# Kernel tuning notes

Hardware: AMD Instinct MI355X
Metric: run time of the kernel (lower is better)

Reference implementation:

```python
import jax, jax.numpy as jnp
from jax import lax
import numpy as np

RADIUS = 0.2
NSAMPLE = 64


def _ball_query(xyz, new_xyz, radius, nsample):
    """Faithful PointNet++ ball query.

    For each center, take the first `nsample` point indices (in index order)
    whose squared distance < radius^2; if fewer than nsample are found, the
    remaining slots are filled with the first found index (CUDA kernel
    semantics). Returns int32 idx of shape (B, npoint, nsample).
    """
    N = xyz.shape[1]
    # (B, npoint, N) squared distances
    d2 = jnp.sum((new_xyz[:, :, None, :] - xyz[:, None, :, :]) ** 2, axis=-1)
    within = d2 < (radius * radius)
    # key = point index if within ball, else N (sentinel); smallest nsample
    # keys == first nsample in-ball indices in index order.
    key = jnp.where(within, jnp.arange(N, dtype=jnp.int32), jnp.int32(N))
    neg_vals, _ = lax.top_k(-key, nsample)          # largest of -key = smallest key
    sel = -neg_vals                                  # (B, npoint, nsample)
    valid = sel < N
    first = jnp.where(valid[..., :1], sel[..., :1], 0)  # first found idx (or 0)
    return jnp.where(valid, sel, first)


def _group_gather(features, idx):
    # features: (B, C, N), idx: (B, npoint, nsample) -> (B, C, npoint, nsample)
    return jax.vmap(lambda f, i: f[:, i])(features, idx)


def setup_inputs() -> dict:
    key = jax.random.key(0)
    k1, k2, k3 = jax.random.split(key, 3)
    B, N, npoint, C = 4, 16384, 2048, 64
    xyz = jax.random.uniform(k1, (B, N, 3), dtype=jnp.float32)
    new_xyz = jax.random.uniform(k2, (B, npoint, 3), dtype=jnp.float32)
    features = jax.random.normal(k3, (B, C, N), dtype=jnp.float32)
    return {"xyz": xyz, "new_xyz": new_xyz, "features": features}


def reference(xyz, new_xyz, features):
    idx = _ball_query(xyz, new_xyz, RADIUS, NSAMPLE)          # (B, npoint, nsample)
    xyz_t = jnp.transpose(xyz, (0, 2, 1))                      # (B, 3, N)
    grouped_xyz = _group_gather(xyz_t, idx)                    # (B, 3, npoint, nsample)
    grouped_xyz = grouped_xyz - jnp.transpose(new_xyz, (0, 2, 1))[..., None]
    grouped_features = _group_gather(features, idx)            # (B, C, npoint, nsample)
    new_features = jnp.concatenate([grouped_xyz, grouped_features], axis=1)
    # original code does .transpose(1, 2) -> (B, npoint, 3+C, nsample)
    return jnp.transpose(new_features, (0, 2, 1, 3))
```

## Files before the change

kernel.cpp:

```cpp
#include <hip/hip_runtime.h>


#define BB 4
#define NN 16384
#define NP 2048
#define CC 64
#define NS 64
#define CH (3 + CC)
#define NCHUNK (NN / 256)
#define ST 65

typedef float f32x4 __attribute__((ext_vector_type(4)));

__global__ __launch_bounds__(256) void pn2_transpose_kernel(
    const float* __restrict__ f, float* __restrict__ ft)
{
    __shared__ float tile[CC][65];
    const int g = blockIdx.x;
    const int xcd = g & 7;
    const int b = xcd >> 1;
    const int tidx = ((xcd & 1) << 7) + (g >> 3);
    const int n0 = tidx << 6;
    const int col = threadIdx.x & 63;
    const int r4  = threadIdx.x >> 6;
    const float* src = f + (size_t)b * CC * NN;
#pragma unroll
    for (int i = 0; i < 16; ++i) {
        const int c = r4 + i * 4;
        tile[c][col] = __builtin_nontemporal_load(&src[(size_t)c * NN + n0 + col]);
    }
    __syncthreads();
    float* dst = ft + ((size_t)b * NN + n0) * CC;
#pragma unroll
    for (int i = 0; i < 16; ++i) {
        const int n = r4 + i * 4;
        dst[(size_t)n * CC + col] = tile[col][n];
    }
}

__global__ __launch_bounds__(256, 4) void pn2_qg_kernel(
    const float* __restrict__ xyz,
    const float* __restrict__ new_xyz,
    const float* __restrict__ ft,
    float* __restrict__ out)
{
    __shared__ int sidx[4][NS];
    __shared__ float stile[4][32 * ST];

    const int lane = threadIdx.x & 63;
    const int wave = threadIdx.x >> 6;

    const int g = blockIdx.x;
    const int xcd = g & 7;
    const int cg = ((xcd >> 1) << 9) + ((xcd & 1) << 8) + (g >> 3);
    const int center = cg * 4 + wave;
    const int b = center >> 11;
    const int j = center & (NP - 1);

    const float r2 = 0.04f;
    const float* q = new_xyz + ((size_t)b * NP + j) * 3;
    const float cx = q[0], cy = q[1], cz = q[2];

    const float* xb = xyz + (size_t)b * NN * 3;
    const float4* x4 = (const float4*)xb;
    int* widx = sidx[wave];

    const int base = 3 * lane;
    const unsigned long long low = (1ull << lane) - 1ull;
    int found = 0;
    int it = 0;
    float4 A = x4[base], Bv = x4[base + 1], Cv = x4[base + 2];

    while (true) {
        const int nit = (it + 1 < NCHUNK) ? it + 1 : it;
        const size_t nb = (size_t)nit * 192 + base;
        float4 nA = x4[nb], nB = x4[nb + 1], nC = x4[nb + 2];

        const int n0 = it * 256 + 4 * lane;
        const float px[4] = {A.x, A.w, Bv.z, Cv.y};
        const float py[4] = {A.y, Bv.x, Bv.w, Cv.z};
        const float pz[4] = {A.z, Bv.y, Cv.x, Cv.w};
        bool in[4];
        unsigned long long m[4];
#pragma unroll
        for (int k = 0; k < 4; ++k) {
            const float dx = px[k] - cx;
            const float dy = py[k] - cy;
            const float dz = pz[k] - cz;
            const float d2 = __fadd_rn(__fadd_rn(__fmul_rn(dx, dx), __fmul_rn(dy, dy)),
                                       __fmul_rn(dz, dz));
            in[k] = d2 < r2;
            m[k] = __ballot(in[k]);
        }
        int pos = found
                + (int)__popcll(m[0] & low) + (int)__popcll(m[1] & low)
                + (int)__popcll(m[2] & low) + (int)__popcll(m[3] & low);
#pragma unroll
        for (int k = 0; k < 4; ++k) {
            if (in[k]) {
                if (pos < NS) widx[pos] = n0 + k;
                ++pos;
            }
        }
        found += (int)(__popcll(m[0]) + __popcll(m[1])
                     + __popcll(m[2]) + __popcll(m[3]));
        if (found >= NS || it == NCHUNK - 1) break;
        A = nA; Bv = nB; Cv = nC; ++it;
    }

    int myidx = 0;
    if (found > 0) {
        const int first = widx[0];
        myidx = (lane < found) ? widx[lane] : first;
    }
    widx[lane] = myidx;

    const float* pp = xb + (size_t)myidx * 3;
    float* ob = out + (size_t)center * CH * NS;
    __builtin_nontemporal_store(pp[0] - cx, ob + 0 * NS + lane);
    __builtin_nontemporal_store(pp[1] - cy, ob + 1 * NS + lane);
    __builtin_nontemporal_store(pp[2] - cz, ob + 2 * NS + lane);

    const float* ftb = ft + (size_t)b * NN * CC;
    float* tw = stile[wave];
    const int sub  = lane & 15;
    const int rsub = lane >> 4;
    const int sq   = lane & 7;
    const int cc8  = lane >> 3;

#pragma unroll
    for (int h = 0; h < 2; ++h) {
        int ridx[8];
#pragma unroll
        for (int i = 0; i < 8; ++i) ridx[i] = widx[32 * h + 4 * i + rsub];
        float4 v[8];
#pragma unroll
        for (int i = 0; i < 8; ++i)
            v[i] = *(const float4*)(ftb + (size_t)ridx[i] * CC + 4 * sub);
#pragma unroll
        for (int i = 0; i < 8; ++i) {
            float* tr = tw + (4 * i + rsub) * ST + 4 * sub;
            tr[0] = v[i].x; tr[1] = v[i].y; tr[2] = v[i].z; tr[3] = v[i].w;
        }
#pragma unroll
        for (int t = 0; t < 8; ++t) {
            const int c = 8 * t + cc8;
            f32x4 u;
            u.x = tw[(4 * sq + 0) * ST + c];
            u.y = tw[(4 * sq + 1) * ST + c];
            u.z = tw[(4 * sq + 2) * ST + c];
            u.w = tw[(4 * sq + 3) * ST + c];
            float* o = ob + (size_t)(3 + c) * NS + 32 * h + 4 * sq;
            __builtin_nontemporal_store(u, (f32x4*)o);
        }
    }
}

__global__ __launch_bounds__(256, 4) void pn2_group_kernel(
    const float* __restrict__ xyz, const float* __restrict__ new_xyz,
    const float* __restrict__ features, float* __restrict__ out)
{
    __shared__ int sidx[4][NS];
    const int lane = threadIdx.x & 63;
    const int wave = threadIdx.x >> 6;
    const int center = blockIdx.x * 4 + wave;
    const int b = center >> 11;
    const int j = center & (NP - 1);
    const float r2 = 0.04f;
    const float* q = new_xyz + ((size_t)b * NP + j) * 3;
    const float cx = q[0], cy = q[1], cz = q[2];
    int* widx = sidx[wave];
    int found = 0;
    for (int it = 0; it < NN / 64; ++it) {
        const int n = it * 64 + lane;
        const float* p = xyz + ((size_t)b * NN + n) * 3;
        const float dx = p[0] - cx, dy = p[1] - cy, dz = p[2] - cz;
        const float d2 = __fadd_rn(__fadd_rn(__fmul_rn(dx, dx), __fmul_rn(dy, dy)),
                                   __fmul_rn(dz, dz));
        const bool within = d2 < r2;
        const unsigned long long mask = __ballot(within);
        const int pos = found + (int)__popcll(mask & ((1ull << lane) - 1ull));
        if (within && pos < NS) widx[pos] = n;
        found += (int)__popcll(mask);
        if (found >= NS) break;
    }
    int myidx = 0;
    if (found > 0) {
        const int first = widx[0];
        myidx = (lane < found) ? widx[lane] : first;
    }
    const float* pp = xyz + ((size_t)b * NN + myidx) * 3;
    float* ob = out + (((size_t)b * NP + j) * (size_t)CH) * NS + lane;
    ob[0 * NS] = pp[0] - cx;
    ob[1 * NS] = pp[1] - cy;
    ob[2 * NS] = pp[2] - cz;
    const float* fb = features + (size_t)b * CC * NN + myidx;
#pragma unroll 8
    for (int c = 0; c < CC; ++c) ob[(size_t)(3 + c) * NS] = fb[(size_t)c * NN];
}

extern "C" void kernel_launch(void* const* d_in, const int* in_sizes, int n_in,
                              void* d_out, int out_size, void* d_ws, size_t ws_size,
                              hipStream_t stream) {
    const float* xyz      = (const float*)d_in[0];
    const float* new_xyz  = (const float*)d_in[1];
    const float* features = (const float*)d_in[2];
    float* out = (float*)d_out;

    const size_t ft_bytes = (size_t)BB * NN * CC * sizeof(float);

    if (ws_size >= ft_bytes) {
        float* ft = (float*)d_ws;
        pn2_transpose_kernel<<<BB * 256, 256, 0, stream>>>(features, ft);
        pn2_qg_kernel<<<BB * NP / 4, 256, 0, stream>>>(xyz, new_xyz, ft, out);
    } else {
        pn2_group_kernel<<<BB * NP / 4, 256, 0, stream>>>(xyz, new_xyz, features, out);
    }
}
```

Baseline: 46.09 us.

## Run ball query concurrently with feature transpose, then gather in separate kernel

Merges the feature transpose and the ball-query search into one prep kernel whose blocks split between the two roles, so the latency-bound search overlaps the bandwidth-bound transpose. The found indices go to a workspace buffer, and a second kernel reads them back to gather transposed features into the output. This removes the serial dependency of the whole search on the transpose. It adds an idx buffer round trip through global memory, and the prep kernel's blocks now carry mixed workloads.

```diff
diff --git a/kernel.cpp b/kernel.cpp
--- a/kernel.cpp
+++ b/kernel.cpp
@@ -12,50 +12,49 @@
 
 typedef float f32x4 __attribute__((ext_vector_type(4)));
 
-__global__ __launch_bounds__(256) void pn2_transpose_kernel(
-    const float* __restrict__ f, float* __restrict__ ft)
+__global__ __launch_bounds__(256) void pn2_prep_kernel(
+    const float* __restrict__ xyz,
+    const float* __restrict__ new_xyz,
+    const float* __restrict__ features,
+    float* __restrict__ ft,
+    int* __restrict__ idxbuf,
+    float* __restrict__ out)
 {
     __shared__ float tile[CC][65];
+    __shared__ int sidx[4][NS];
+
     const int g = blockIdx.x;
     const int xcd = g & 7;
+    const int r = g >> 3;
     const int b = xcd >> 1;
-    const int tidx = ((xcd & 1) << 7) + (g >> 3);
-    const int n0 = tidx << 6;
-    const int col = threadIdx.x & 63;
-    const int r4  = threadIdx.x >> 6;
-    const float* src = f + (size_t)b * CC * NN;
-#pragma unroll
-    for (int i = 0; i < 16; ++i) {
-        const int c = r4 + i * 4;
-        tile[c][col] = __builtin_nontemporal_load(&src[(size_t)c * NN + n0 + col]);
-    }
-    __syncthreads();
-    float* dst = ft + ((size_t)b * NN + n0) * CC;
-#pragma unroll
-    for (int i = 0; i < 16; ++i) {
-        const int n = r4 + i * 4;
-        dst[(size_t)n * CC + col] = tile[col][n];
-    }
-}
-
-__global__ __launch_bounds__(256, 4) void pn2_qg_kernel(
-    const float* __restrict__ xyz,
-    const float* __restrict__ new_xyz,
-    const float* __restrict__ ft,
-    float* __restrict__ out)
-{
-    __shared__ int sidx[4][NS];
-    __shared__ float stile[4][32 * ST];
+    const int h = xcd & 1;
+
+    if (r < 128) {
+        const int t = h * 128 + r;
+        const int n0 = t << 6;
+        const int col = threadIdx.x & 63;
+        const int r4  = threadIdx.x >> 6;
+        const float* src = features + (size_t)b * CC * NN;
+#pragma unroll
+        for (int i = 0; i < 16; ++i) {
+            const int c = r4 + i * 4;
+            tile[c][col] = __builtin_nontemporal_load(&src[(size_t)c * NN + n0 + col]);
+        }
+        __syncthreads();
+        float* dst = ft + ((size_t)b * NN + n0) * CC;
+#pragma unroll
+        for (int i = 0; i < 16; ++i) {
+            const int n = r4 + i * 4;
+            dst[(size_t)n * CC + col] = tile[col][n];
+        }
+        return;
+    }
 
     const int lane = threadIdx.x & 63;
     const int wave = threadIdx.x >> 6;
-
-    const int g = blockIdx.x;
-    const int xcd = g & 7;
-    const int cg = ((xcd >> 1) << 9) + ((xcd & 1) << 8) + (g >> 3);
-    const int center = cg * 4 + wave;
-    const int b = center >> 11;
-    const int j = center & (NP - 1);
+    const int grp = h * 256 + (r - 128);
+    const int j = grp * 4 + wave;
+    const int center = b * NP + j;
 
     const float r2 = 0.04f;
     const float* q = new_xyz + ((size_t)b * NP + j) * 3;
@@ -113,26 +112,50 @@
         const int first = widx[0];
         myidx = (lane < found) ? widx[lane] : first;
     }
-    widx[lane] = myidx;
+    idxbuf[(size_t)center * NS + lane] = myidx;
 
     const float* pp = xb + (size_t)myidx * 3;
     float* ob = out + (size_t)center * CH * NS;
     __builtin_nontemporal_store(pp[0] - cx, ob + 0 * NS + lane);
     __builtin_nontemporal_store(pp[1] - cy, ob + 1 * NS + lane);
     __builtin_nontemporal_store(pp[2] - cz, ob + 2 * NS + lane);
+}
+
+__global__ __launch_bounds__(256, 4) void pn2_gather_kernel(
+    const float* __restrict__ ft,
+    const int* __restrict__ idxbuf,
+    float* __restrict__ out)
+{
+    __shared__ int sidx[4][NS];
+    __shared__ float stile[4][32 * ST];
+
+    const int g = blockIdx.x;
+    const int xcd = g & 7;
+    const int r = g >> 3;
+    const int b = xcd >> 1;
+    const int h = xcd & 1;
+
+    const int lane = threadIdx.x & 63;
+    const int wave = threadIdx.x >> 6;
+    const int j = (h * 256 + r) * 4 + wave;
+    const int center = b * NP + j;
+
+    int* widx = sidx[wave];
+    widx[lane] = idxbuf[(size_t)center * NS + lane];
 
     const float* ftb = ft + (size_t)b * NN * CC;
     float* tw = stile[wave];
+    float* ob = out + (size_t)center * CH * NS;
     const int sub  = lane & 15;
     const int rsub = lane >> 4;
     const int sq   = lane & 7;
     const int cc8  = lane >> 3;
 
 #pragma unroll
-    for (int h = 0; h < 2; ++h) {
+    for (int hh = 0; hh < 2; ++hh) {
         int ridx[8];
 #pragma unroll
-        for (int i = 0; i < 8; ++i) ridx[i] = widx[32 * h + 4 * i + rsub];
+        for (int i = 0; i < 8; ++i) ridx[i] = widx[32 * hh + 4 * i + rsub];
         float4 v[8];
 #pragma unroll
         for (int i = 0; i < 8; ++i)
@@ -150,7 +173,7 @@
             u.y = tw[(4 * sq + 1) * ST + c];
             u.z = tw[(4 * sq + 2) * ST + c];
             u.w = tw[(4 * sq + 3) * ST + c];
-            float* o = ob + (size_t)(3 + c) * NS + 32 * h + 4 * sq;
+            float* o = ob + (size_t)(3 + c) * NS + 32 * hh + 4 * sq;
             __builtin_nontemporal_store(u, (f32x4*)o);
         }
     }
@@ -207,12 +230,15 @@
     const float* features = (const float*)d_in[2];
     float* out = (float*)d_out;
 
-    const size_t ft_bytes = (size_t)BB * NN * CC * sizeof(float);
-
-    if (ws_size >= ft_bytes) {
-        float* ft = (float*)d_ws;
-        pn2_transpose_kernel<<<BB * 256, 256, 0, stream>>>(features, ft);
-        pn2_qg_kernel<<<BB * NP / 4, 256, 0, stream>>>(xyz, new_xyz, ft, out);
+    const size_t ft_bytes  = (size_t)BB * NN * CC * sizeof(float);
+    const size_t idx_bytes = (size_t)BB * NP * NS * sizeof(int);
+
+    if (ws_size >= ft_bytes + idx_bytes) {
+        float* ft   = (float*)d_ws;
+        int* idxbuf = (int*)((char*)d_ws + ft_bytes);
+        pn2_prep_kernel<<<3072, 256, 0, stream>>>(xyz, new_xyz, features,
+                                                  ft, idxbuf, out);
+        pn2_gather_kernel<<<2048, 256, 0, stream>>>(ft, idxbuf, out);
     } else {
         pn2_group_kernel<<<BB * NP / 4, 256, 0, stream>>>(xyz, new_xyz, features, out);
     }
```

Result: slower. 54.60 us (+18.5%).

## Share xyz chunk loads across block waves through LDS staging

Applied to the files above, without the earlier changes.

All four waves in a block now load each 256-point xyz chunk cooperatively into shared memory once, instead of every wave loading it separately. Each wave then scans the points from LDS, and the block leaves the loop only when every wave has collected its samples. The aim is to cut redundant global/L2 traffic for xyz, in exchange for two block barriers per chunk. Waves that finish early now wait for the slowest wave in the block, which may add latency.

```diff
diff --git a/kernel.cpp b/kernel.cpp
--- a/kernel.cpp
+++ b/kernel.cpp
@@ -45,10 +45,12 @@
     float* __restrict__ out)
 {
     __shared__ int sidx[4][NS];
-    __shared__ float stile[4][32 * ST];
-
-    const int lane = threadIdx.x & 63;
-    const int wave = threadIdx.x >> 6;
+    __shared__ int sdone[4];
+    __shared__ __align__(16) float stile[4][32 * ST];
+
+    const int tid = threadIdx.x;
+    const int lane = tid & 63;
+    const int wave = tid >> 6;
 
     const int g = blockIdx.x;
     const int xcd = g & 7;
@@ -64,48 +66,48 @@
     const float* xb = xyz + (size_t)b * NN * 3;
     const float4* x4 = (const float4*)xb;
     int* widx = sidx[wave];
-
-    const int base = 3 * lane;
+    float* xyzbuf = &stile[0][0];
+    float4* xb4 = (float4*)xyzbuf;
+
+    if (tid < 4) sdone[tid] = 0;
+
     const unsigned long long low = (1ull << lane) - 1ull;
     int found = 0;
+    bool mydone = false;
     int it = 0;
-    float4 A = x4[base], Bv = x4[base + 1], Cv = x4[base + 2];
+    float4 reg;
+    if (tid < 192) reg = x4[tid];
 
     while (true) {
-        const int nit = (it + 1 < NCHUNK) ? it + 1 : it;
-        const size_t nb = (size_t)nit * 192 + base;
-        float4 nA = x4[nb], nB = x4[nb + 1], nC = x4[nb + 2];
-
-        const int n0 = it * 256 + 4 * lane;
-        const float px[4] = {A.x, A.w, Bv.z, Cv.y};
-        const float py[4] = {A.y, Bv.x, Bv.w, Cv.z};
-        const float pz[4] = {A.z, Bv.y, Cv.x, Cv.w};
-        bool in[4];
-        unsigned long long m[4];
-#pragma unroll
-        for (int k = 0; k < 4; ++k) {
-            const float dx = px[k] - cx;
-            const float dy = py[k] - cy;
-            const float dz = pz[k] - cz;
-            const float d2 = __fadd_rn(__fadd_rn(__fmul_rn(dx, dx), __fmul_rn(dy, dy)),
-                                       __fmul_rn(dz, dz));
-            in[k] = d2 < r2;
-            m[k] = __ballot(in[k]);
-        }
-        int pos = found
-                + (int)__popcll(m[0] & low) + (int)__popcll(m[1] & low)
-                + (int)__popcll(m[2] & low) + (int)__popcll(m[3] & low);
-#pragma unroll
-        for (int k = 0; k < 4; ++k) {
-            if (in[k]) {
-                if (pos < NS) widx[pos] = n0 + k;
-                ++pos;
+        __syncthreads();
+        if (it == NCHUNK ||
+            (sdone[0] + sdone[1] + sdone[2] + sdone[3]) == 4) break;
+        if (tid < 192) {
+            xb4[tid] = reg;
+            const int nit = (it + 1 < NCHUNK) ? (it + 1) : it;
+            reg = x4[(size_t)nit * 192 + tid];
+        }
+        __syncthreads();
+        if (!mydone) {
+#pragma unroll
+            for (int k = 0; k < 4; ++k) {
+                const int p = k * 64 + lane;
+                const float dx = xyzbuf[3 * p + 0] - cx;
+                const float dy = xyzbuf[3 * p + 1] - cy;
+                const float dz = xyzbuf[3 * p + 2] - cz;
+                const float d2 = __fadd_rn(__fadd_rn(__fmul_rn(dx, dx),
+                                                     __fmul_rn(dy, dy)),
+                                           __fmul_rn(dz, dz));
+                const bool within = d2 < r2;
+                const unsigned long long m = __ballot(within);
+                const int pos = found + (int)__popcll(m & low);
+                if (within && pos < NS) widx[pos] = it * 256 + p;
+                found += (int)__popcll(m);
             }
-        }
-        found += (int)(__popcll(m[0]) + __popcll(m[1])
-                     + __popcll(m[2]) + __popcll(m[3]));
-        if (found >= NS || it == NCHUNK - 1) break;
-        A = nA; Bv = nB; Cv = nC; ++it;
+            if (found >= NS) mydone = true;
+            if (lane == 0) sdone[wave] = mydone ? 1 : 0;
+        }
+        ++it;
     }
 
     int myidx = 0;
```

Result: slower. 59.47 us (+29.0%).

## Use one-wave blocks per center with double-buffered prefetch and smaller LDS tiles

Applied to the files above, without the earlier changes.

The query-and-group kernel now launches one 64-thread block per center instead of four centers per 256-thread block. The xyz scan prefetches two chunks ahead with alternating register sets. The feature transpose works on 16-row quarter tiles over two LDS buffers, which cuts shared memory per block and should allow more resident waves per CU. The tradeoffs are more blocks to schedule and more vector registers for the second prefetch buffer.

```diff
diff --git a/kernel.cpp b/kernel.cpp
--- a/kernel.cpp
+++ b/kernel.cpp
@@ -38,24 +38,22 @@
     }
 }
 
-__global__ __launch_bounds__(256, 4) void pn2_qg_kernel(
+__global__ __launch_bounds__(64, 4) void pn2_qg_kernel(
     const float* __restrict__ xyz,
     const float* __restrict__ new_xyz,
     const float* __restrict__ ft,
     float* __restrict__ out)
 {
-    __shared__ int sidx[4][NS];
-    __shared__ float stile[4][32 * ST];
-
-    const int lane = threadIdx.x & 63;
-    const int wave = threadIdx.x >> 6;
+    __shared__ int widx[NS];
+    __shared__ __align__(16) float stile[2][16 * ST];
+
+    const int lane = threadIdx.x;
 
     const int g = blockIdx.x;
     const int xcd = g & 7;
-    const int cg = ((xcd >> 1) << 9) + ((xcd & 1) << 8) + (g >> 3);
-    const int center = cg * 4 + wave;
-    const int b = center >> 11;
-    const int j = center & (NP - 1);
+    const int b = xcd >> 1;
+    const int j = ((xcd & 1) << 10) + (g >> 3);
+    const int center = b * NP + j;
 
     const float r2 = 0.04f;
     const float* q = new_xyz + ((size_t)b * NP + j) * 3;
@@ -63,50 +61,68 @@
 
     const float* xb = xyz + (size_t)b * NN * 3;
     const float4* x4 = (const float4*)xb;
-    int* widx = sidx[wave];
 
     const int base = 3 * lane;
     const unsigned long long low = (1ull << lane) - 1ull;
     int found = 0;
     int it = 0;
-    float4 A = x4[base], Bv = x4[base + 1], Cv = x4[base + 2];
+
+    float4 A0 = x4[base],       B0 = x4[base + 1],       C0 = x4[base + 2];
+    float4 A1 = x4[192 + base], B1 = x4[192 + base + 1], C1 = x4[192 + base + 2];
+
+#define QPROC(Ar, Br, Cr)                                                      \
+    {                                                                          \
+        const int n0 = it * 256 + 4 * lane;                                    \
+        const float px[4] = {Ar.x, Ar.w, Br.z, Cr.y};                          \
+        const float py[4] = {Ar.y, Br.x, Br.w, Cr.z};                          \
+        const float pz[4] = {Ar.z, Br.y, Cr.x, Cr.w};                          \
+        bool in[4];                                                            \
+        unsigned long long m[4];                                               \
+        _Pragma("unroll")                                                      \
+        for (int k = 0; k < 4; ++k) {                                          \
+            const float dx = px[k] - cx;                                       \
+            const float dy = py[k] - cy;                                       \
+            const float dz = pz[k] - cz;                                       \
+                    \
+            const float d2 = __fadd_rn(__fadd_rn(__fmul_rn(dx, dx),            \
+                                                 __fmul_rn(dy, dy)),           \
+                                       __fmul_rn(dz, dz));                     \
+            in[k] = d2 < r2;                                                   \
+            m[k] = __ballot(in[k]);                                            \
+        }                                                                      \
+        int pos = found                                                        \
+                + (int)__popcll(m[0] & low) + (int)__popcll(m[1] & low)        \
+                + (int)__popcll(m[2] & low) + (int)__popcll(m[3] & low);       \
+        _Pragma("unroll")                                                      \
+        for (int k = 0; k < 4; ++k) {                                          \
+            if (in[k]) {                                                       \
+                if (pos < NS) widx[pos] = n0 + k;                              \
+                ++pos;                                                         \
+            }                                                                  \
+        }                                                                      \
+        found += (int)(__popcll(m[0]) + __popcll(m[1])                         \
+                     + __popcll(m[2]) + __popcll(m[3]));                       \
+    }
 
     while (true) {
-        const int nit = (it + 1 < NCHUNK) ? it + 1 : it;
-        const size_t nb = (size_t)nit * 192 + base;
-        float4 nA = x4[nb], nB = x4[nb + 1], nC = x4[nb + 2];
-
-        const int n0 = it * 256 + 4 * lane;
-        const float px[4] = {A.x, A.w, Bv.z, Cv.y};
-        const float py[4] = {A.y, Bv.x, Bv.w, Cv.z};
-        const float pz[4] = {A.z, Bv.y, Cv.x, Cv.w};
-        bool in[4];
-        unsigned long long m[4];
-#pragma unroll
-        for (int k = 0; k < 4; ++k) {
-            const float dx = px[k] - cx;
-            const float dy = py[k] - cy;
-            const float dz = pz[k] - cz;
-            const float d2 = __fadd_rn(__fadd_rn(__fmul_rn(dx, dx), __fmul_rn(dy, dy)),
-                                       __fmul_rn(dz, dz));
-            in[k] = d2 < r2;
-            m[k] = __ballot(in[k]);
-        }
-        int pos = found
-                + (int)__popcll(m[0] & low) + (int)__popcll(m[1] & low)
-                + (int)__popcll(m[2] & low) + (int)__popcll(m[3] & low);
-#pragma unroll
-        for (int k = 0; k < 4; ++k) {
-            if (in[k]) {
-                if (pos < NS) widx[pos] = n0 + k;
-                ++pos;
-            }
-        }
-        found += (int)(__popcll(m[0]) + __popcll(m[1])
-                     + __popcll(m[2]) + __popcll(m[3]));
+        QPROC(A0, B0, C0)
         if (found >= NS || it == NCHUNK - 1) break;
-        A = nA; Bv = nB; Cv = nC; ++it;
-    }
+        {
+            const int nit = (it + 2 < NCHUNK) ? it + 2 : it;
+            const size_t nb = (size_t)nit * 192 + base;
+            A0 = x4[nb]; B0 = x4[nb + 1]; C0 = x4[nb + 2];
+        }
+        ++it;
+        QPROC(A1, B1, C1)
+        if (found >= NS || it == NCHUNK - 1) break;
+        {
+            const int nit = (it + 2 < NCHUNK) ? it + 2 : it;
+            const size_t nb = (size_t)nit * 192 + base;
+            A1 = x4[nb]; B1 = x4[nb + 1]; C1 = x4[nb + 2];
+        }
+        ++it;
+    }
+#undef QPROC
 
     int myidx = 0;
     if (found > 0) {
@@ -122,35 +138,35 @@
     __builtin_nontemporal_store(pp[2] - cz, ob + 2 * NS + lane);
 
     const float* ftb = ft + (size_t)b * NN * CC;
-    float* tw = stile[wave];
     const int sub  = lane & 15;
     const int rsub = lane >> 4;
-    const int sq   = lane & 7;
-    const int cc8  = lane >> 3;
-
-#pragma unroll
-    for (int h = 0; h < 2; ++h) {
-        int ridx[8];
-#pragma unroll
-        for (int i = 0; i < 8; ++i) ridx[i] = widx[32 * h + 4 * i + rsub];
-        float4 v[8];
-#pragma unroll
-        for (int i = 0; i < 8; ++i)
+    const int sq4  = lane & 3;
+    const int c16  = lane >> 2;
+
+#pragma unroll
+    for (int qt = 0; qt < 4; ++qt) {
+        float* tw = stile[qt & 1];
+        int ridx[4];
+#pragma unroll
+        for (int i = 0; i < 4; ++i) ridx[i] = widx[16 * qt + 4 * i + rsub];
+        float4 v[4];
+#pragma unroll
+        for (int i = 0; i < 4; ++i)
             v[i] = *(const float4*)(ftb + (size_t)ridx[i] * CC + 4 * sub);
 #pragma unroll
-        for (int i = 0; i < 8; ++i) {
+        for (int i = 0; i < 4; ++i) {
             float* tr = tw + (4 * i + rsub) * ST + 4 * sub;
             tr[0] = v[i].x; tr[1] = v[i].y; tr[2] = v[i].z; tr[3] = v[i].w;
         }
 #pragma unroll
-        for (int t = 0; t < 8; ++t) {
-            const int c = 8 * t + cc8;
+        for (int t = 0; t < 4; ++t) {
+            const int c = 16 * t + c16;
             f32x4 u;
-            u.x = tw[(4 * sq + 0) * ST + c];
-            u.y = tw[(4 * sq + 1) * ST + c];
-            u.z = tw[(4 * sq + 2) * ST + c];
-            u.w = tw[(4 * sq + 3) * ST + c];
-            float* o = ob + (size_t)(3 + c) * NS + 32 * h + 4 * sq;
+            u.x = tw[(4 * sq4 + 0) * ST + c];
+            u.y = tw[(4 * sq4 + 1) * ST + c];
+            u.z = tw[(4 * sq4 + 2) * ST + c];
+            u.w = tw[(4 * sq4 + 3) * ST + c];
+            float* o = ob + (size_t)(3 + c) * NS + 16 * qt + 4 * sq4;
             __builtin_nontemporal_store(u, (f32x4*)o);
         }
     }
@@ -212,7 +228,7 @@
     if (ws_size >= ft_bytes) {
         float* ft = (float*)d_ws;
         pn2_transpose_kernel<<<BB * 256, 256, 0, stream>>>(features, ft);
-        pn2_qg_kernel<<<BB * NP / 4, 256, 0, stream>>>(xyz, new_xyz, ft, out);
+        pn2_qg_kernel<<<BB * NP, 64, 0, stream>>>(xyz, new_xyz, ft, out);
     } else {
         pn2_group_kernel<<<BB * NP / 4, 256, 0, stream>>>(xyz, new_xyz, features, out);
     }
```

Measured after the change: 67.47 us. +46.4%, slower.
